# Kernel optimization log

Measured on AMD Instinct MI355X. Metric: run time of the kernel, lower is better.

Reference implementation:

```python
import jax, jax.numpy as jnp
import numpy as np

D_MODEL = 32
NHEAD = 4
NUM_LAYERS = 4
WINDOW = 256
D_FF = 2 * D_MODEL
INPUT_DIM = 58
MAX_DEPTH = 12
HEAD_OUT = 25


def _layernorm(x, g, b, eps=1e-5):
    m = jnp.mean(x, axis=-1, keepdims=True)
    v = jnp.mean((x - m) ** 2, axis=-1, keepdims=True)
    return (x - m) / jnp.sqrt(v + eps) * g + b


def _layer(h, ipw, ipb, opw, opb, g1, b1, w1, bb1, w2, bb2, g2, b2):
    # Post-norm transformer layer (subclass overrides parent's norm_first path).
    Wn, S, D = h.shape
    dh = D // NHEAD
    qkv = h @ ipw.T + ipb                      # [Wn, S, 3D]
    q, k, v = jnp.split(qkv, 3, axis=-1)
    q = q.reshape(Wn, S, NHEAD, dh).transpose(0, 2, 1, 3)  # [Wn,H,S,dh]
    k = k.reshape(Wn, S, NHEAD, dh).transpose(0, 2, 1, 3)
    v = v.reshape(Wn, S, NHEAD, dh).transpose(0, 2, 1, 3)
    scores = jnp.einsum('whqd,whkd->whqk', q, k) / jnp.sqrt(jnp.asarray(dh, h.dtype))
    a = jax.nn.softmax(scores, axis=-1)        # eager attn weights (need_weights=True path)
    o = jnp.einsum('whqk,whkd->whqd', a, v).transpose(0, 2, 1, 3).reshape(Wn, S, D)
    o = o @ opw.T + opb
    h = _layernorm(h + o, g1, b1)
    ff = jax.nn.gelu(h @ w1.T + bb1, approximate=False) @ w2.T + bb2
    return _layernorm(h + ff, g2, b2)


def setup_inputs() -> dict:
    key = jax.random.key(0)
    ks = jax.random.split(key, 24)
    B, N = 2, 65536
    x = jax.random.uniform(ks[0], (B, N, INPUT_DIM), dtype=jnp.float32)
    layers = jax.random.randint(ks[1], (B, N), 0, MAX_DEPTH)

    def w(k, shape, s=0.05):
        return jax.random.normal(k, shape, jnp.float32) * s

    L = NUM_LAYERS
    return dict(
        x=x,
        layers=layers,
        feature_proj_w=w(ks[2], (D_MODEL, INPUT_DIM)),
        feature_proj_b=w(ks[3], (D_MODEL,)),
        layer_embed=w(ks[4], (MAX_DEPTH, D_MODEL)),
        fourier_B=jax.random.normal(ks[5], (3, D_MODEL // 2), jnp.float32) * 1024.0,
        in_proj_w=w(ks[6], (L, 3 * D_MODEL, D_MODEL)),
        in_proj_b=w(ks[7], (L, 3 * D_MODEL)),
        out_proj_w=w(ks[8], (L, D_MODEL, D_MODEL)),
        out_proj_b=w(ks[9], (L, D_MODEL)),
        ln1_g=jnp.ones((L, D_MODEL), jnp.float32),
        ln1_b=jnp.zeros((L, D_MODEL), jnp.float32),
        lin1_w=w(ks[10], (L, D_FF, D_MODEL)),
        lin1_b=w(ks[11], (L, D_FF)),
        lin2_w=w(ks[12], (L, D_MODEL, D_FF)),
        lin2_b=w(ks[13], (L, D_MODEL)),
        ln2_g=jnp.ones((L, D_MODEL), jnp.float32),
        ln2_b=jnp.zeros((L, D_MODEL), jnp.float32),
        norm_out_g=jnp.ones((D_MODEL,), jnp.float32),
        norm_out_b=jnp.zeros((D_MODEL,), jnp.float32),
        head_w=w(ks[14], (HEAD_OUT, D_MODEL)),
        head_b=w(ks[15], (HEAD_OUT,)),
    )


def reference(x, layers, feature_proj_w, feature_proj_b, layer_embed, fourier_B,
              in_proj_w, in_proj_b, out_proj_w, out_proj_b,
              ln1_g, ln1_b, lin1_w, lin1_b, lin2_w, lin2_b, ln2_g, ln2_b,
              norm_out_g, norm_out_b, head_w, head_b):
    B, N, _ = x.shape
    pos = x[:, :, :3]
    proj = (2.0 * jnp.pi) * (pos @ fourier_B)                  # [B,N,D/2]
    pe = jnp.concatenate([jnp.sin(proj), jnp.cos(proj)], axis=-1)
    h = x @ feature_proj_w.T + feature_proj_b + layer_embed[layers] + pe
    # N chosen divisible by WINDOW, so pad_len == 0 (original pads otherwise)
    nw = N // WINDOW
    h = h.reshape(B * nw, WINDOW, D_MODEL)
    for i in range(NUM_LAYERS):
        h = _layer(h, in_proj_w[i], in_proj_b[i], out_proj_w[i], out_proj_b[i],
                   ln1_g[i], ln1_b[i], lin1_w[i], lin1_b[i], lin2_w[i], lin2_b[i],
                   ln2_g[i], ln2_b[i])
    h = h.reshape(B, N, D_MODEL)
    return _layernorm(h, norm_out_g, norm_out_b) @ head_w.T + head_b
```

## Files before the change

kernel.cpp:

```cpp
#include <hip/hip_runtime.h>

constexpr int S    = 256;
constexpr int D    = 32;
constexpr int NH   = 4;
constexpr int DH   = 8;
constexpr int DFF  = 64;
constexpr int NL   = 4;
constexpr int IND  = 58;
constexpr int HOUT = 25;
constexpr int TPB  = 256;

typedef float  f2 __attribute__((ext_vector_type(2)));
typedef float  f4 __attribute__((ext_vector_type(4)));
typedef __fp16 h2 __attribute__((ext_vector_type(2)));
typedef __fp16 h4 __attribute__((ext_vector_type(4)));
typedef __fp16 h8 __attribute__((ext_vector_type(8)));

__device__ __forceinline__ f4 MFMA16(h4 a, h4 b, f4 c) {
  return __builtin_amdgcn_mfma_f32_16x16x16f16(a, b, c, 0, 0, 0);
}
__device__ __forceinline__ f4 MFMA32(h8 a, h8 b, f4 c) {
  return __builtin_amdgcn_mfma_f32_16x16x32_f16(a, b, c, 0, 0, 0);
}
__device__ __forceinline__ h8 hcat(h4 a, h4 b) {
  return __builtin_shufflevector(a, b, 0, 1, 2, 3, 4, 5, 6, 7);
}

constexpr int HOFF  = 0;
constexpr int VOFF  = 16384;
constexpr int QOFF  = 32768;
constexpr int LDSSZ = 49152;

__device__ __forceinline__ unsigned pk2(float a, float b) {
  h2 h = __builtin_amdgcn_cvt_pkrtz(a, b);
  return __builtin_bit_cast(unsigned, h);
}

__device__ __forceinline__ float exp2fast(float x) {
#if __has_builtin(__builtin_amdgcn_exp2f)
  return __builtin_amdgcn_exp2f(x);
#else
  return exp2f(x);
#endif
}

__device__ __forceinline__ void wave_fence() {
  __builtin_amdgcn_wave_barrier();
}

template<int NF2>
__device__ __forceinline__ float dotp(const float* __restrict__ w,
                                      const float* __restrict__ v) {
  const f2* W = (const f2*)w;
  const f2* V = (const f2*)v;
  f2 a0 = {0.f, 0.f}, a1 = {0.f, 0.f};
#pragma unroll
  for (int i = 0; i < NF2; i += 2) a0 += V[i] * W[i];
#pragma unroll
  for (int i = 1; i < NF2; i += 2) a1 += V[i] * W[i];
  f2 s = a0 + a1;
  return s.x + s.y;
}

__device__ __forceinline__ float gelu(float x) {
  float u = 2.3022082f * fmaf(0.044715f * x * x, x, x);
  return x * __builtin_amdgcn_rcpf(1.0f + exp2fast(-u));
}

__device__ __forceinline__ void lnorm(float* h, const float* __restrict__ g,
                                      const float* __restrict__ b) {
  f2* hv = (f2*)h;
  f2 s0 = hv[0], s1 = hv[1];
#pragma unroll
  for (int i = 2; i < 16; i += 2) { s0 += hv[i]; s1 += hv[i + 1]; }
  f2 s = s0 + s1;
  const float m = (s.x + s.y) * (1.0f / D);
  const f2 m2 = {m, m};
  f2 v0 = {0.f, 0.f}, v1 = {0.f, 0.f};
#pragma unroll
  for (int i = 0; i < 16; i += 2) {
    f2 c0 = hv[i] - m2;     v0 += c0 * c0;
    f2 c1 = hv[i + 1] - m2; v1 += c1 * c1;
  }
  f2 vs = v0 + v1;
  const float inv = __builtin_amdgcn_rsqf((vs.x + vs.y) * (1.0f / D) + 1e-5f);
  const f2 inv2 = {inv, inv};
  const f2 mi2 = {-m * inv, -m * inv};
  const f2* g2 = (const f2*)g;
  const f2* b2 = (const f2*)b;
#pragma unroll
  for (int i = 0; i < 16; ++i) {
    f2 t = hv[i] * inv2 + mi2;
    hv[i] = t * g2[i] + b2[i];
  }
}

__device__ __forceinline__ void embed_token(
    const float* __restrict__ xrow, int lay,
    const float* __restrict__ fpw, const float* __restrict__ fpb,
    const float* __restrict__ lemb, const float* __restrict__ fB,
    float* __restrict__ h) {
  float xr[IND];
  const f2* xv = (const f2*)xrow;
#pragma unroll
  for (int i = 0; i < 29; ++i) { f2 t = xv[i]; xr[2 * i] = t.x; xr[2 * i + 1] = t.y; }
  const float* le = lemb + lay * D;
  float pe[D];
#pragma unroll
  for (int k = 0; k < 16; ++k) {
    float t = xr[0] * fB[k] + xr[1] * fB[16 + k] + xr[2] * fB[32 + k];
#if __has_builtin(__builtin_amdgcn_sinf) && __has_builtin(__builtin_amdgcn_cosf) && __has_builtin(__builtin_amdgcn_fractf)
    float u = __builtin_amdgcn_fractf(t);
    pe[k]      = __builtin_amdgcn_sinf(u);
    pe[16 + k] = __builtin_amdgcn_cosf(u);
#else
    float sv, cv;
    sincosf(6.2831853071795864f * (t - floorf(t)), &sv, &cv);
    pe[k] = sv; pe[16 + k] = cv;
#endif
  }
#pragma unroll
  for (int d = 0; d < D; ++d)
    h[d] = dotp<29>(fpw + d * IND, xr) + fpb[d] + le[d] + pe[d];
}

__device__ __forceinline__ h4 bfrag(const float* __restrict__ W, int row,
                                    int K, int kh, int quad) {
  f4 w = *(const f4*)(W + row * K + kh * 16 + quad * 4);
  uint2 p{pk2(w.x, w.y), pk2(w.z, w.w)};
  return __builtin_bit_cast(h4, p);
}
__device__ __forceinline__ h8 bfrag8(const float* __restrict__ W, int row,
                                     int quad) {
  return hcat(bfrag(W, row, 32, 0, quad), bfrag(W, row, 32, 1, quad));
}
__device__ __forceinline__ h8 wfrag8(const float* __restrict__ W, int row,
                                     int quad, float sc) {
  f4 w0 = *(const f4*)(W + row * D + quad * 4) * sc;
  f4 w1 = *(const f4*)(W + row * D + 16 + quad * 4) * sc;
  uint2 p0{pk2(w0.x, w0.y), pk2(w0.z, w0.w)};
  uint2 p1{pk2(w1.x, w1.y), pk2(w1.z, w1.w)};
  return hcat(__builtin_bit_cast(h4, p0), __builtin_bit_cast(h4, p1));
}
__device__ __forceinline__ h4 afrag32(const unsigned char* sm, int base,
                                      int tok, int kh, int quad) {
  return *(const h4*)(sm + base + tok * 64 + (((kh * 4 + quad) ^ (tok & 7)) * 8));
}
__device__ __forceinline__ h8 afrag8(const unsigned char* sm, int base,
                                     int tok, int quad) {
  return hcat(afrag32(sm, base, tok, 0, quad), afrag32(sm, base, tok, 1, quad));
}

__device__ __forceinline__ void store_h16(unsigned char* sm, int tok,
                                          const float* __restrict__ h) {
#pragma unroll
  for (int c = 0; c < 8; ++c) {
    uint2 p{pk2(h[4 * c], h[4 * c + 1]), pk2(h[4 * c + 2], h[4 * c + 3])};
    *(uint2*)(sm + HOFF + tok * 64 + ((c ^ (tok & 7)) * 8)) = p;
  }
}
__device__ __forceinline__ void add_row32(const unsigned char* sm, int base,
                                          int tok, float* __restrict__ h) {
  f2* hv = (f2*)h;
#pragma unroll
  for (int c = 0; c < 8; ++c) {
    h4 q = *(const h4*)(sm + base + tok * 64 + ((c ^ (tok & 7)) * 8));
    f2 lo = {(float)q[0], (float)q[1]};
    f2 hi = {(float)q[2], (float)q[3]};
    hv[2 * c] += lo;
    hv[2 * c + 1] += hi;
  }
}

__global__ void __launch_bounds__(TPB, 2)
spai_fused(const float* __restrict__ x,    const int*   __restrict__ layers,
           const float* __restrict__ fpw,  const float* __restrict__ fpb,
           const float* __restrict__ lemb, const float* __restrict__ fB,
           const float* __restrict__ ipw,  const float* __restrict__ ipb,
           const float* __restrict__ opw,  const float* __restrict__ opb,
           const float* __restrict__ ln1g, const float* __restrict__ ln1b,
           const float* __restrict__ w1,   const float* __restrict__ b1,
           const float* __restrict__ w2,   const float* __restrict__ b2,
           const float* __restrict__ ln2g, const float* __restrict__ ln2b,
           const float* __restrict__ nog,  const float* __restrict__ nob,
           const float* __restrict__ hw,   const float* __restrict__ hb,
           float* __restrict__ out) {
  __shared__ __align__(16) unsigned char sm[LDSSZ];
  const int tid    = threadIdx.x;
  const int lane   = tid & 63;
  const int wave   = tid >> 6;
  const int n16    = lane & 15;
  const int quad   = lane >> 4;
  const int pairi  = wave >> 1;
  const int parity = wave & 1;
  const int qbank  = QOFF + pairi * 8192;
  const size_t blk_tok = (size_t)blockIdx.x * S;

  float h[D];
  embed_token(x + (blk_tok + tid) * IND, layers[blk_tok + tid],
              fpw, fpb, lemb, fB, h);
  store_h16(sm, tid, h);

  for (int l = 0; l < NL; ++l) {
    __syncthreads();

    const float* Wi = ipw + l * (3 * D) * D;
    const float* Bi = ipb + l * (3 * D);

    h4 Kf[16], Vf[16];
    {
      const float scq = 0.51006973f;
      h8 BfQ = wfrag8(Wi, pairi * 16 + n16, quad, scq);
      h8 BfK = wfrag8(Wi + 32 * D, pairi * 16 + n16, quad, 1.0f);
      h8 BfV = wfrag8(Wi + 64 * D, pairi * 16 + n16, quad, 1.0f);
      f4 bq = *(const f4*)(Bi + pairi * 16 + quad * 4) * scq;
      f4 bk = *(const f4*)(Bi + 32 + pairi * 16 + quad * 4);
      const float bvv = Bi[64 + pairi * 16 + n16];
      const f4 bv4 = {bvv, bvv, bvv, bvv};
      const unsigned fill = (n16 == 8) ? 0x3C003C00u : 0u;
      const int qsw = (n16 >> 2) & 3;
#pragma unroll
      for (int it = 0; it < 16; ++it) {
        const int tok = it * 16 + n16;
        h8 Ah = afrag8(sm, HOFF, tok, quad);
        f4 Cq = MFMA32(BfQ, Ah, bq);
        f4 Ck = MFMA32(BfK, Ah, bk);
        f4 Cv = MFMA32(Ah, BfV, bv4);
        uint2 q{pk2(Cq[0], Cq[1]), pk2(Cq[2], Cq[3])};
        *(uint2*)(sm + qbank + tok * 32 + ((quad ^ qsw) * 8)) = q;
        uint2 kk{pk2(Ck[0], Ck[1]), pk2(Ck[2], Ck[3])};
        Kf[it] = __builtin_bit_cast(h4, kk);
        uint2 v{pk2(Cv[0], Cv[1]), pk2(Cv[2], Cv[3])};
        if (parity) {
          v.x = (unsigned)__shfl_xor((int)v.x, 8);
          v.y = (unsigned)__shfl_xor((int)v.y, 8);
        }
        if (n16 >= 8) { v.x = fill; v.y = fill; }
        Vf[it] = __builtin_bit_cast(h4, v);
      }
    }
    wave_fence();

    {
      const int hh  = wave;
      const int m   = n16;
      const int msw = m & 7;
      const int ooff = VOFF + (((hh * 2 + quad) ^ msw) * 8);
      const int qrd  = qbank + ((quad ^ ((m >> 2) & 3)) * 8);
      const bool qdead = (quad >> 1) != parity;
      const f4 Z = {0.f, 0.f, 0.f, 0.f};
#pragma unroll 4
      for (int it = 0; it < 16; ++it) {
        const int ti = it * 16 + m;
        uint2 qv = *(const uint2*)(sm + qrd + ti * 32);
        if (qdead) { qv.x = 0u; qv.y = 0u; }
        h4 Qf = __builtin_bit_cast(h4, qv);
        f4 Of0 = Z, Of1 = Z;
#pragma unroll
        for (int j2 = 0; j2 < 8; ++j2) {
          f4 T0 = MFMA16(Kf[2 * j2], Qf, Z);
          f4 T1 = MFMA16(Kf[2 * j2 + 1], Qf, Z);
          uint2 pa{pk2(exp2fast(T0[0]), exp2fast(T0[1])),
                   pk2(exp2fast(T0[2]), exp2fast(T0[3]))};
          uint2 pb{pk2(exp2fast(T1[0]), exp2fast(T1[1])),
                   pk2(exp2fast(T1[2]), exp2fast(T1[3]))};
          h8 P8 = hcat(__builtin_bit_cast(h4, pa), __builtin_bit_cast(h4, pb));
          h8 V8 = hcat(Vf[2 * j2], Vf[2 * j2 + 1]);
          if (j2 & 1) Of1 = MFMA32(V8, P8, Of1);
          else        Of0 = MFMA32(V8, P8, Of0);
        }
        f4 Of = Of0 + Of1;
        float rinv = __builtin_amdgcn_rcpf(Of[0]);
        rinv = __builtin_bit_cast(
            float, __builtin_amdgcn_ds_bpermute(
                       (32 + m) << 2, __builtin_bit_cast(int, rinv)));
        if (quad < 2) {
          f4 o = Of * rinv;
          uint2 p{pk2(o[0], o[1]), pk2(o[2], o[3])};
          *(uint2*)(sm + ooff + ti * 64) = p;
        }
      }
    }
    __syncthreads();

    {
      const float* Wo = opw + l * D * D;
      const float* Bo = opb + l * D;
      h8 WoF[2]; f4 bo2[2];
#pragma unroll
      for (int nt = 0; nt < 2; ++nt) {
        bo2[nt] = *(const f4*)(Bo + nt * 16 + quad * 4);
        WoF[nt] = bfrag8(Wo, nt * 16 + n16, quad);
      }
      const int kswz = n16 & 7;
#pragma unroll
      for (int ii = 0; ii < 4; ++ii) {
        const int tok = (wave * 4 + ii) * 16 + n16;
        h8 A8 = afrag8(sm, VOFF, tok, quad);
#pragma unroll
        for (int nt = 0; nt < 2; ++nt) {
          f4 C = MFMA32(WoF[nt], A8, bo2[nt]);
          uint2 p{pk2(C[0], C[1]), pk2(C[2], C[3])};
          *(uint2*)(sm + VOFF + tok * 64 + (((nt * 4 + quad) ^ kswz) * 8)) = p;
        }
      }
    }
    wave_fence();

    add_row32(sm, VOFF, tid, h);
    lnorm(h, ln1g + l * D, ln1b + l * D);
    store_h16(sm, tid, h);
    wave_fence();

    {
      const float* Wa = w1 + l * DFF * D;
      const float* Ba = b1 + l * DFF;
      const float* Wb = w2 + l * D * DFF;
      const float* Bb = b2 + l * D;
      h8 WaF[4]; f4 ba4[4]; h8 WbF[4]; f4 bb2[2];
#pragma unroll
      for (int ft = 0; ft < 4; ++ft) {
        ba4[ft] = *(const f4*)(Ba + ft * 16 + quad * 4);
        WaF[ft] = bfrag8(Wa, ft * 16 + n16, quad);
      }
#pragma unroll
      for (int nt = 0; nt < 2; ++nt) {
        bb2[nt] = *(const f4*)(Bb + nt * 16 + quad * 4);
#pragma unroll
        for (int g = 0; g < 2; ++g)
          WbF[nt * 2 + g] = hcat(bfrag(Wb, nt * 16 + n16, 64, 2 * g, quad),
                                 bfrag(Wb, nt * 16 + n16, 64, 2 * g + 1, quad));
      }
      const int kswz = n16 & 7;
#pragma unroll
      for (int tt = 0; tt < 4; ++tt) {
        const int tok = (wave * 4 + tt) * 16 + n16;
        h8 A8 = afrag8(sm, HOFF, tok, quad);
        h4 Pf[4];
#pragma unroll
        for (int ft = 0; ft < 4; ++ft) {
          f4 C = MFMA32(WaF[ft], A8, ba4[ft]);
          uint2 p{pk2(gelu(C[0]), gelu(C[1])), pk2(gelu(C[2]), gelu(C[3]))};
          Pf[ft] = __builtin_bit_cast(h4, p);
        }
        h8 P8a = hcat(Pf[0], Pf[1]);
        h8 P8b = hcat(Pf[2], Pf[3]);
#pragma unroll
        for (int nt = 0; nt < 2; ++nt) {
          f4 C = MFMA32(WbF[nt * 2], P8a, bb2[nt]);
          C = MFMA32(WbF[nt * 2 + 1], P8b, C);
          uint2 p{pk2(C[0], C[1]), pk2(C[2], C[3])};
          *(uint2*)(sm + VOFF + tok * 64 + (((nt * 4 + quad) ^ kswz) * 8)) = p;
        }
      }
    }
    wave_fence();

    add_row32(sm, VOFF, tid, h);
    lnorm(h, ln2g + l * D, ln2b + l * D);
    if (l < NL - 1) store_h16(sm, tid, h);
  }

  __syncthreads();
  lnorm(h, nog, nob);
  float* hs = (float*)sm;
#pragma unroll
  for (int o = 0; o < HOUT; ++o)
    hs[tid * HOUT + o] = dotp<16>(hw + o * D, h) + hb[o];
  __syncthreads();
  f2* og = (f2*)(out + blk_tok * HOUT);
  const f2* os2 = (const f2*)hs;
  for (int i = tid; i < S * HOUT / 2; i += TPB) og[i] = os2[i];
}

extern "C" void kernel_launch(void* const* d_in, const int* in_sizes, int n_in,
                              void* d_out, int out_size, void* d_ws, size_t ws_size,
                              hipStream_t stream) {
  const float* x    = (const float*)d_in[0];
  const int*   lays = (const int*)  d_in[1];
  const float* fpw  = (const float*)d_in[2];
  const float* fpb  = (const float*)d_in[3];
  const float* lemb = (const float*)d_in[4];
  const float* fB   = (const float*)d_in[5];
  const float* ipw  = (const float*)d_in[6];
  const float* ipb  = (const float*)d_in[7];
  const float* opw  = (const float*)d_in[8];
  const float* opb  = (const float*)d_in[9];
  const float* ln1g = (const float*)d_in[10];
  const float* ln1b = (const float*)d_in[11];
  const float* w1   = (const float*)d_in[12];
  const float* b1   = (const float*)d_in[13];
  const float* w2   = (const float*)d_in[14];
  const float* b2   = (const float*)d_in[15];
  const float* ln2g = (const float*)d_in[16];
  const float* ln2b = (const float*)d_in[17];
  const float* nog  = (const float*)d_in[18];
  const float* nob  = (const float*)d_in[19];
  const float* hw   = (const float*)d_in[20];
  const float* hb   = (const float*)d_in[21];
  float* out = (float*)d_out;

  const int nwin = in_sizes[0] / (S * IND);
  spai_fused<<<nwin, TPB, 0, stream>>>(x, lays, fpw, fpb, lemb, fB, ipw, ipb,
                                       opw, opb, ln1g, ln1b, w1, b1, w2, b2,
                                       ln2g, ln2b, nog, nob, hw, hb, out);
}
```

Before: 238.1 us.

## Keep Q fragments in registers instead of LDS, permute V weights at load

Q projections are now held in per-wave registers (Qf[16]) instead of being written to a swizzled LDS bank and read back in the attention loop. This drops the Q bank and cuts LDS from 48KB to 32KB. The V lane swap is moved into the weight-row index, removing the shuffles. The attention loop is fully unrolled and wrapped in s_setprio to favour MFMA issue. The extra 16 h4 registers per thread raise register pressure and may lower occupancy, which could offset the lower LDS use.

```diff
diff --git a/kernel.cpp b/kernel.cpp
--- a/kernel.cpp
+++ b/kernel.cpp
@@ -28,8 +28,7 @@
 
 constexpr int HOFF  = 0;
 constexpr int VOFF  = 16384;
-constexpr int QOFF  = 32768;
-constexpr int LDSSZ = 49152;
+constexpr int LDSSZ = 32768;
 
 __device__ __forceinline__ unsigned pk2(float a, float b) {
   h2 h = __builtin_amdgcn_cvt_pkrtz(a, b);
@@ -193,7 +192,6 @@
   const int quad   = lane >> 4;
   const int pairi  = wave >> 1;
   const int parity = wave & 1;
-  const int qbank  = QOFF + pairi * 8192;
   const size_t blk_tok = (size_t)blockIdx.x * S;
 
   float h[D];
@@ -207,18 +205,19 @@
     const float* Wi = ipw + l * (3 * D) * D;
     const float* Bi = ipb + l * (3 * D);
 
-    h4 Kf[16], Vf[16];
+    h4 Kf[16], Vf[16], Qf[16];
     {
       const float scq = 0.51006973f;
       h8 BfQ = wfrag8(Wi, pairi * 16 + n16, quad, scq);
       h8 BfK = wfrag8(Wi + 32 * D, pairi * 16 + n16, quad, 1.0f);
-      h8 BfV = wfrag8(Wi + 64 * D, pairi * 16 + n16, quad, 1.0f);
+      const int vrow = pairi * 16 + (n16 ^ (parity << 3));
+      h8 BfV = wfrag8(Wi + 64 * D, vrow, quad, 1.0f);
       f4 bq = *(const f4*)(Bi + pairi * 16 + quad * 4) * scq;
       f4 bk = *(const f4*)(Bi + 32 + pairi * 16 + quad * 4);
-      const float bvv = Bi[64 + pairi * 16 + n16];
+      const float bvv = Bi[64 + vrow];
       const f4 bv4 = {bvv, bvv, bvv, bvv};
       const unsigned fill = (n16 == 8) ? 0x3C003C00u : 0u;
-      const int qsw = (n16 >> 2) & 3;
+      const bool qlive = (quad >> 1) == parity;
 #pragma unroll
       for (int it = 0; it < 16; ++it) {
         const int tok = it * 16 + n16;
@@ -227,39 +226,32 @@
         f4 Ck = MFMA32(BfK, Ah, bk);
         f4 Cv = MFMA32(Ah, BfV, bv4);
         uint2 q{pk2(Cq[0], Cq[1]), pk2(Cq[2], Cq[3])};
-        *(uint2*)(sm + qbank + tok * 32 + ((quad ^ qsw) * 8)) = q;
+        if (!qlive) { q.x = 0u; q.y = 0u; }
+        Qf[it] = __builtin_bit_cast(h4, q);
         uint2 kk{pk2(Ck[0], Ck[1]), pk2(Ck[2], Ck[3])};
         Kf[it] = __builtin_bit_cast(h4, kk);
         uint2 v{pk2(Cv[0], Cv[1]), pk2(Cv[2], Cv[3])};
-        if (parity) {
-          v.x = (unsigned)__shfl_xor((int)v.x, 8);
-          v.y = (unsigned)__shfl_xor((int)v.y, 8);
-        }
         if (n16 >= 8) { v.x = fill; v.y = fill; }
         Vf[it] = __builtin_bit_cast(h4, v);
       }
     }
-    wave_fence();
 
     {
       const int hh  = wave;
       const int m   = n16;
       const int msw = m & 7;
       const int ooff = VOFF + (((hh * 2 + quad) ^ msw) * 8);
-      const int qrd  = qbank + ((quad ^ ((m >> 2) & 3)) * 8);
-      const bool qdead = (quad >> 1) != parity;
       const f4 Z = {0.f, 0.f, 0.f, 0.f};
-#pragma unroll 4
+#pragma unroll
       for (int it = 0; it < 16; ++it) {
         const int ti = it * 16 + m;
-        uint2 qv = *(const uint2*)(sm + qrd + ti * 32);
-        if (qdead) { qv.x = 0u; qv.y = 0u; }
-        h4 Qf = __builtin_bit_cast(h4, qv);
+        h4 Q4 = Qf[it];
+        __builtin_amdgcn_s_setprio(1);
         f4 Of0 = Z, Of1 = Z;
 #pragma unroll
         for (int j2 = 0; j2 < 8; ++j2) {
-          f4 T0 = MFMA16(Kf[2 * j2], Qf, Z);
-          f4 T1 = MFMA16(Kf[2 * j2 + 1], Qf, Z);
+          f4 T0 = MFMA16(Kf[2 * j2], Q4, Z);
+          f4 T1 = MFMA16(Kf[2 * j2 + 1], Q4, Z);
           uint2 pa{pk2(exp2fast(T0[0]), exp2fast(T0[1])),
                    pk2(exp2fast(T0[2]), exp2fast(T0[3]))};
           uint2 pb{pk2(exp2fast(T1[0]), exp2fast(T1[1])),
@@ -270,6 +262,7 @@
           else        Of0 = MFMA32(V8, P8, Of0);
         }
         f4 Of = Of0 + Of1;
+        __builtin_amdgcn_s_setprio(0);
         float rinv = __builtin_amdgcn_rcpf(Of[0]);
         rinv = __builtin_bit_cast(
             float, __builtin_amdgcn_ds_bpermute(
```

Result: no change. 235.8 us (-1.0%).
